# Kernel optimization log

Measured on AMD Instinct MI355X. Metric: run time of the kernel, lower is better.

Reference implementation:

```python
import jax, jax.numpy as jnp
import numpy as np

NEG_BIG = -9.0e15  # matches torch's -9000000000000000.0 mask fill
ALPHA = 0.2        # LeakyReLU negative slope


def setup_inputs() -> dict:
    key = jax.random.key(0)
    k1, k2, k3, k4 = jax.random.split(key, 4)
    bs, N, F_in, F_out = 4, 4096, 512, 64
    x = jax.random.normal(k1, (bs, N, F_in), dtype=jnp.float32)
    adj = jax.random.randint(k2, (N, N), 0, 2, dtype=jnp.int32)
    # xavier_uniform with gain=1.414
    lim_W = 1.414 * np.sqrt(6.0 / (F_in + F_out))
    W = jax.random.uniform(k3, (F_in, F_out), minval=-lim_W, maxval=lim_W, dtype=jnp.float32)
    lim_a = 1.414 * np.sqrt(6.0 / (2 * F_out + 1))
    a = jax.random.uniform(k4, (2 * F_out, 1), minval=-lim_a, maxval=lim_a, dtype=jnp.float32)
    return {"x": x, "adj": adj, "W": W, "a": a}


def reference(x, adj, W, a):
    # h = x @ W : [bs, N, F_out]
    h = jnp.einsum('bnf,fo->bno', x, W)
    F_out = W.shape[1]
    a1, a2 = a[:F_out, 0], a[F_out:, 0]  # each [F_out]
    # e_ij = LeakyReLU(a1.Wh_i + a2.Wh_j) -- same math as the O(N^2*2F) concat
    s1 = jnp.einsum('bno,o->bn', h, a1)  # [bs, N]
    s2 = jnp.einsum('bno,o->bn', h, a2)  # [bs, N]
    e = s1[:, :, None] + s2[:, None, :]  # [bs, N, N]
    e = jax.nn.leaky_relu(e, negative_slope=ALPHA)
    mask = (adj > 0)[None, :, :]
    attention = jnp.where(mask, e, NEG_BIG)
    attention = jax.nn.softmax(attention, axis=-1)
    # dropout is identity in eval mode (p applied only during training)
    h_prime = jnp.einsum('bij,bjo->bio', attention, h)
    return jax.nn.elu(h_prime)  # concat=True path
```

## Files before the change

kernel.cpp:

```cpp
#include <hip/hip_runtime.h>

#define LOG2E 1.4426950408889634f

typedef __attribute__((ext_vector_type(8))) short short8;
typedef __attribute__((ext_vector_type(4))) float f32x4;
using u32 = unsigned int;
using u16 = unsigned short;
using u64 = unsigned long long;

__global__ __launch_bounds__(256) void prep_kernel(const int* __restrict__ adj,
                                                   u32* __restrict__ mask_t,
                                                   const float* __restrict__ W,
                                                   u16* __restrict__ wt) {
    if (blockIdx.x >= 2048) {
        int t = (blockIdx.x - 2048) * 256 + threadIdx.x;
        int n = t >> 7, k4 = (t & 127) << 2;
        u32 c0 = __float_as_uint(W[(size_t)(k4 + 0) * 64 + n]) + 0x8000u;
        u32 c1 = __float_as_uint(W[(size_t)(k4 + 1) * 64 + n]) + 0x8000u;
        u32 c2 = __float_as_uint(W[(size_t)(k4 + 2) * 64 + n]) + 0x8000u;
        u32 c3 = __float_as_uint(W[(size_t)(k4 + 3) * 64 + n]) + 0x8000u;
        uint2 o;
        o.x = (c0 >> 16) | (c1 & 0xffff0000u);
        o.y = (c2 >> 16) | (c3 & 0xffff0000u);
        *(uint2*)(wt + (size_t)n * 512 + k4) = o;
        return;
    }
    const int wid = (blockIdx.x * 256 + threadIdx.x) >> 6;
    const int lane = threadIdx.x & 63;
    for (int t = wid; t < 65536; t += 8192) {
        const int r = t >> 4, c4 = t & 15;
        const int* base = adj + (size_t)r * 4096 + c4 * 256 + lane;
        int v0 = __builtin_nontemporal_load(base);
        int v1 = __builtin_nontemporal_load(base + 64);
        int v2 = __builtin_nontemporal_load(base + 128);
        int v3 = __builtin_nontemporal_load(base + 192);
        u64 b0 = __ballot(v0 > 0);
        u64 b1 = __ballot(v1 > 0);
        u64 b2 = __ballot(v2 > 0);
        u64 b3 = __ballot(v3 > 0);
        if (lane < 8) {
            u64 bv = (lane & 4) ? ((lane & 2) ? b3 : b2) : ((lane & 2) ? b1 : b0);
            u32 w = (u32)(bv >> ((lane & 1) << 5));
            mask_t[(size_t)(c4 * 8 + lane) * 4096 + r] = w;
        }
    }
}

__global__ __launch_bounds__(512) void k1f(const float* __restrict__ x,
                                           const u16* __restrict__ wt,
                                           const float* __restrict__ a,
                                           u16* __restrict__ h_t,
                                           float* __restrict__ s1p,
                                           float* __restrict__ s2p) {
    __shared__ float red[4][16][65];
    const int rt = blockIdx.x, b = blockIdx.y;
    const int tid = threadIdx.x, wave = tid >> 6, lane = tid & 63;
    const int g = wave & 3, kz = wave >> 2;
    const int m = lane & 15, quad = lane >> 4;
    const int row = rt * 64 + g * 16 + m;
    const float* xb = x + ((size_t)b * 4096 + row) * 512 + kz * 256 + quad * 8;
    const u16* wb = wt + (size_t)m * 512 + kz * 256 + quad * 8;

    f32x4 acc[4];
#pragma unroll
    for (int ot = 0; ot < 4; ot++) acc[ot] = (f32x4){0.f, 0.f, 0.f, 0.f};

    union BU { uint4 q; short8 v; };
    float4 ax[2][2];
    BU bw[2][4];
#pragma unroll
    for (int s = 0; s < 2; s++) {
        ax[s][0] = *(const float4*)(xb + s * 32);
        ax[s][1] = *(const float4*)(xb + s * 32 + 4);
#pragma unroll
        for (int ot = 0; ot < 4; ot++)
            bw[s][ot].q = *(const uint4*)(wb + (size_t)ot * 16 * 512 + s * 32);
    }
#pragma unroll
    for (int s = 0; s < 8; s++) {
        const int cur = s & 1;
        union { u32 u[4]; short8 v; } af;
        const float* a0 = (const float*)&ax[cur][0];
#pragma unroll
        for (int p = 0; p < 4; p++) {
            u32 lo = __float_as_uint(a0[2 * p]) + 0x8000u;
            u32 hi = __float_as_uint(a0[2 * p + 1]) + 0x8000u;
            af.u[p] = __builtin_amdgcn_perm(hi, lo, 0x07060302u);
        }
#pragma unroll
        for (int ot = 0; ot < 4; ot++)
            acc[ot] = __builtin_amdgcn_mfma_f32_16x16x32_bf16(af.v, bw[cur][ot].v,
                                                              acc[ot], 0, 0, 0);
        if (s + 2 < 8) {
            ax[cur][0] = *(const float4*)(xb + (s + 2) * 32);
            ax[cur][1] = *(const float4*)(xb + (s + 2) * 32 + 4);
#pragma unroll
            for (int ot = 0; ot < 4; ot++)
                bw[cur][ot].q =
                    *(const uint4*)(wb + (size_t)ot * 16 * 512 + (s + 2) * 32);
        }
    }
    if (kz) {
#pragma unroll
        for (int ot = 0; ot < 4; ot++)
#pragma unroll
            for (int r = 0; r < 4; r++)
                red[g][quad * 4 + r][ot * 16 + m] = acc[ot][r];
    }
    __syncthreads();
    if (kz) return;
#pragma unroll
    for (int ot = 0; ot < 4; ot++)
#pragma unroll
        for (int r = 0; r < 4; r++)
            acc[ot][r] += red[g][quad * 4 + r][ot * 16 + m];

    float a1v[4], a2v[4];
#pragma unroll
    for (int ot = 0; ot < 4; ot++) {
        a1v[ot] = a[ot * 16 + m];
        a2v[ot] = a[64 + ot * 16 + m];
    }
    float s1r[4], s2r[4];
#pragma unroll
    for (int r = 0; r < 4; r++) {
        s1r[r] = 0.f; s2r[r] = 0.f;
#pragma unroll
        for (int ot = 0; ot < 4; ot++) {
            s1r[r] = fmaf(acc[ot][r], a1v[ot], s1r[r]);
            s2r[r] = fmaf(acc[ot][r], a2v[ot], s2r[r]);
        }
    }
#pragma unroll
    for (int d = 1; d < 16; d <<= 1) {
#pragma unroll
        for (int r = 0; r < 4; r++) {
            s1r[r] += __shfl_xor(s1r[r], d);
            s2r[r] += __shfl_xor(s2r[r], d);
        }
    }
    if (m == 0) {
#pragma unroll
        for (int r = 0; r < 4; r++) {
            int rr = rt * 64 + g * 16 + quad * 4 + r;
            s1p[b * 4096 + rr] = s1r[r] * LOG2E;
            s2p[b * 4096 + rr] = s2r[r] * LOG2E;
        }
    }
#pragma unroll
    for (int ot = 0; ot < 4; ot++) {
        u32 b0 = __float_as_uint(acc[ot][0]) + 0x8000u;
        u32 b1 = __float_as_uint(acc[ot][1]) + 0x8000u;
        u32 b2 = __float_as_uint(acc[ot][2]) + 0x8000u;
        u32 b3 = __float_as_uint(acc[ot][3]) + 0x8000u;
        uint2 u;
        u.x = (b0 >> 16) | (b1 & 0xffff0000u);
        u.y = (b2 >> 16) | (b3 & 0xffff0000u);
        *(uint2*)(h_t + ((size_t)(b * 64 + ot * 16 + m)) * 4096
                  + rt * 64 + g * 16 + quad * 4) = u;
    }
}

template <int NSTEP>
__global__ __launch_bounds__(256, 8) void k2_attn(const u16* __restrict__ h_t,
                                                  const u32* __restrict__ mask_t,
                                                  const float* __restrict__ s1p,
                                                  const float* __restrict__ s2p,
                                                  u16* __restrict__ part,
                                                  float* __restrict__ lp) {
    constexpr int JSEG = NSTEP * 32;
    constexpr int T = NSTEP / 2;
    __shared__ u16 hB[2][64 * 64];
    __shared__ float s2l[JSEG];
    const int b = blockIdx.y, seg = blockIdx.z, rb = blockIdx.x;
    const int tid = threadIdx.x, wave = tid >> 6, lane = tid & 63;
    const int m = lane & 15, quad = lane >> 4;
    const int row = rb * 64 + wave * 16 + m;
    const int jstart = seg * JSEG;
    const float t1 = s1p[b * 4096 + row];
    const u16* hsrc = h_t + (size_t)b * 64 * 4096 + jstart;
    const u32* mrow = mask_t + (size_t)(jstart >> 5) * 4096 + row;

    for (int t = tid; t < (JSEG >> 2); t += 256)
        ((float4*)s2l)[t] = ((const float4*)(s2p + b * 4096 + jstart))[t];

    f32x4 acc[4], accd;
#pragma unroll
    for (int ot = 0; ot < 4; ot++) acc[ot] = (f32x4){0.f, 0.f, 0.f, 0.f};
    accd = (f32x4){0.f, 0.f, 0.f, 0.f};

    u32 mw[4];
#pragma unroll
    for (int s = 0; s < 4; s++) mw[s] = mrow[(size_t)s * 4096];
    union { u32 u[4]; short8 v; } ones;
#pragma unroll
    for (int p = 0; p < 4; p++) ones.u[p] = 0x3F803F80u;

    const int cj = tid & 7;
    const int ow = tid >> 3;
    uint4 pf[2];
    pf[0] = *(const uint4*)(hsrc + (size_t)ow * 4096 + (cj << 3));
    pf[1] = *(const uint4*)(hsrc + (size_t)(ow + 32) * 4096 + (cj << 3));
    *(uint4*)(hB[0] + (size_t)ow * 64 + ((cj ^ (ow & 7)) << 3)) = pf[0];
    *(uint4*)(hB[0] + (size_t)(ow + 32) * 64 + ((cj ^ ((ow + 32) & 7)) << 3)) = pf[1];
    __syncthreads();

    for (int jt = 0; jt < T; jt++) {
        const int cb = jt & 1;
        if (jt + 1 < T) {
            pf[0] = *(const uint4*)(hsrc + (size_t)ow * 4096 + (jt + 1) * 64 + (cj << 3));
            pf[1] = *(const uint4*)(hsrc + (size_t)(ow + 32) * 4096 + (jt + 1) * 64 + (cj << 3));
        }
#pragma unroll
        for (int ks = 0; ks < 2; ks++) {
            const int s = jt * 2 + ks;
            const u32 mws = mw[s & 3] >> (quad * 8);
            if (s + 4 < NSTEP) mw[(s + 4) & 3] = mrow[(size_t)(s + 4) * 4096];

            const float4 sa = *(const float4*)&s2l[s * 32 + quad * 8];
            const float4 sb = *(const float4*)&s2l[s * 32 + quad * 8 + 4];
            const float sv[8] = {sa.x, sa.y, sa.z, sa.w, sb.x, sb.y, sb.z, sb.w};
            union { u32 u[4]; short8 v; } af;
#pragma unroll
            for (int p = 0; p < 4; p++) {
                float t0 = t1 + sv[2 * p];
                float u0 = fmaxf(t0, 0.2f * t0);
                float w0 = __builtin_amdgcn_exp2f(u0);
                u32 m0 = (u32)(((int)(mws << (31 - 2 * p))) >> 31);
                u32 w0u = __float_as_uint(w0) & m0;
                float t2 = t1 + sv[2 * p + 1];
                float u2 = fmaxf(t2, 0.2f * t2);
                float w1 = __builtin_amdgcn_exp2f(u2);
                u32 m1 = (u32)(((int)(mws << (30 - 2 * p))) >> 31);
                u32 w1u = __float_as_uint(w1) & m1;
                af.u[p] = __builtin_amdgcn_perm(w1u, w0u, 0x07060302u);
            }
            const int jc = ks * 4 + quad;
#pragma unroll
            for (int ot = 0; ot < 4; ot++) {
                const int o = ot * 16 + m;
                short8 bfv = *(const short8*)(hB[cb] + (size_t)o * 64 + ((jc ^ (o & 7)) << 3));
                acc[ot] = __builtin_amdgcn_mfma_f32_16x16x32_bf16(af.v, bfv, acc[ot], 0, 0, 0);
            }
            accd = __builtin_amdgcn_mfma_f32_16x16x32_bf16(af.v, ones.v, accd, 0, 0, 0);
        }
        if (jt + 1 < T) {
            const int nb = cb ^ 1;
            *(uint4*)(hB[nb] + (size_t)ow * 64 + ((cj ^ (ow & 7)) << 3)) = pf[0];
            *(uint4*)(hB[nb] + (size_t)(ow + 32) * 64 + ((cj ^ ((ow + 32) & 7)) << 3)) = pf[1];
        }
        __syncthreads();
    }
    u16* pb = part + (((size_t)(seg * 4 + b) * 4096) + rb * 64 + wave * 16) * 64;
#pragma unroll
    for (int ot = 0; ot < 4; ot++)
#pragma unroll
        for (int r = 0; r < 4; r++) {
            u32 v = __float_as_uint(acc[ot][r]) + 0x8000u;
            pb[(quad * 4 + r) * 64 + ot * 16 + m] = (u16)(v >> 16);
        }
    if (m == 0) {
        float* lpb = lp + (size_t)(seg * 4 + b) * 4096 + rb * 64 + wave * 16 + quad * 4;
#pragma unroll
        for (int r = 0; r < 4; r++) lpb[r] = accd[r];
    }
}

template <int S>
__global__ __launch_bounds__(256) void k3_fin(const u16* __restrict__ part,
                                              const float* __restrict__ lp,
                                              float* __restrict__ out) {
    int idx = blockIdx.x * 256 + threadIdx.x;
    int o4 = (idx & 15) << 2;
    int bi = idx >> 4;
    uint2 pv[S];
    float lv[S];
#pragma unroll
    for (int s = 0; s < S; s++) {
        pv[s] = *(const uint2*)&part[((size_t)s * 16384 + bi) * 64 + o4];
        lv[s] = lp[(size_t)s * 16384 + bi];
    }
    float p0 = 0.f, p1 = 0.f, p2 = 0.f, p3 = 0.f, l = 0.f;
#pragma unroll
    for (int s = 0; s < S; s++) {
        p0 += __uint_as_float(pv[s].x << 16);
        p1 += __uint_as_float(pv[s].x & 0xffff0000u);
        p2 += __uint_as_float(pv[s].y << 16);
        p3 += __uint_as_float(pv[s].y & 0xffff0000u);
        l += lv[s];
    }
    float rl = 1.f / l;
    p0 *= rl; p1 *= rl; p2 *= rl; p3 *= rl;
    float4 o;
    o.x = p0 > 0.f ? p0 : __builtin_amdgcn_exp2f(p0 * LOG2E) - 1.f;
    o.y = p1 > 0.f ? p1 : __builtin_amdgcn_exp2f(p1 * LOG2E) - 1.f;
    o.z = p2 > 0.f ? p2 : __builtin_amdgcn_exp2f(p2 * LOG2E) - 1.f;
    o.w = p3 > 0.f ? p3 : __builtin_amdgcn_exp2f(p3 * LOG2E) - 1.f;
    *(float4*)&out[(size_t)bi * 64 + o4] = o;
}

extern "C" void kernel_launch(void* const* d_in, const int* in_sizes, int n_in,
                              void* d_out, int out_size, void* d_ws, size_t ws_size,
                              hipStream_t stream) {
    const float* x  = (const float*)d_in[0];
    const int* adj  = (const int*)d_in[1];
    const float* W  = (const float*)d_in[2];
    const float* a  = (const float*)d_in[3];
    float* out = (float*)d_out;
    char* ws = (char*)d_ws;

    u16* h_t   = (u16*)ws;
    u32* maskt = (u32*)(ws + (2 << 20));
    float* s1p = (float*)(ws + (4 << 20));
    float* s2p = s1p + 16384;
    float* lp  = s2p + 16384;
    size_t base = (4u << 20) + 2 * 65536;
    int S = 8;
    while (S > 1 && base + (size_t)S * (65536 + 2097152) + 65536 > ws_size) S >>= 1;
    u16* part = (u16*)(ws + base + (size_t)S * 65536);
    u16* wtp = (u16*)(ws + base + (size_t)S * 65536 + (size_t)S * 2097152);

    prep_kernel<<<2080, 256, 0, stream>>>(adj, maskt, W, wtp);
    k1f<<<dim3(64, 4), 512, 0, stream>>>(x, wtp, a, h_t, s1p, s2p);
    if (S == 8)      k2_attn<16><<<dim3(64, 4, 8), 256, 0, stream>>>(h_t, maskt, s1p, s2p, part, lp);
    else if (S == 4) k2_attn<32><<<dim3(64, 4, 4), 256, 0, stream>>>(h_t, maskt, s1p, s2p, part, lp);
    else if (S == 2) k2_attn<64><<<dim3(64, 4, 2), 256, 0, stream>>>(h_t, maskt, s1p, s2p, part, lp);
    else             k2_attn<128><<<dim3(64, 4, 1), 256, 0, stream>>>(h_t, maskt, s1p, s2p, part, lp);
    if (S == 8)      k3_fin<8><<<1024, 256, 0, stream>>>(part, lp, out);
    else if (S == 4) k3_fin<4><<<1024, 256, 0, stream>>>(part, lp, out);
    else if (S == 2) k3_fin<2><<<1024, 256, 0, stream>>>(part, lp, out);
    else             k3_fin<1><<<1024, 256, 0, stream>>>(part, lp, out);
}
```

Baseline: 161.6 us.

## Fuse prep with projection GEMM and fold split-K finalize into attention via tickets

Merges the adjacency mask packing, the W bf16 conversion and the x@W projection into a single kernel. Each block now computes one 16-column slice of h from a swizzled LDS copy of W, writing partial s1/s2 scores per column quarter. The separate finalize kernel is removed: the last attention segment block for each row tile, chosen by an atomic ticket counter, sums the partials, normalises and applies ELU. This cuts two launches and overlaps the mask work with the GEMM, at the cost of redundant W loads per block, four-way partial reads of s1/s2, and a serialized tail in the last-arriving blocks.

```diff
diff --git a/kernel.cpp b/kernel.cpp
--- a/kernel.cpp
+++ b/kernel.cpp
@@ -8,76 +8,69 @@
 using u16 = unsigned short;
 using u64 = unsigned long long;
 
-__global__ __launch_bounds__(256) void prep_kernel(const int* __restrict__ adj,
-                                                   u32* __restrict__ mask_t,
-                                                   const float* __restrict__ W,
-                                                   u16* __restrict__ wt) {
-    if (blockIdx.x >= 2048) {
-        int t = (blockIdx.x - 2048) * 256 + threadIdx.x;
-        int n = t >> 7, k4 = (t & 127) << 2;
-        u32 c0 = __float_as_uint(W[(size_t)(k4 + 0) * 64 + n]) + 0x8000u;
-        u32 c1 = __float_as_uint(W[(size_t)(k4 + 1) * 64 + n]) + 0x8000u;
-        u32 c2 = __float_as_uint(W[(size_t)(k4 + 2) * 64 + n]) + 0x8000u;
-        u32 c3 = __float_as_uint(W[(size_t)(k4 + 3) * 64 + n]) + 0x8000u;
-        uint2 o;
-        o.x = (c0 >> 16) | (c1 & 0xffff0000u);
-        o.y = (c2 >> 16) | (c3 & 0xffff0000u);
-        *(uint2*)(wt + (size_t)n * 512 + k4) = o;
+__global__ __launch_bounds__(256, 8) void fused_prep(
+        const float* __restrict__ x, const int* __restrict__ adj,
+        const float* __restrict__ W, const float* __restrict__ a,
+        u16* __restrict__ h_t, u32* __restrict__ mask_t,
+        float* __restrict__ s1part, float* __restrict__ s2part,
+        int* __restrict__ cnt) {
+    __shared__ u16 wq[16 * 512];
+    const int bx = blockIdx.x;
+    const int tid = threadIdx.x;
+
+    if (bx >= 1024) {
+        if (bx == 1024 && tid < 256) cnt[tid] = 0;
+        const int wid = ((bx - 1024) << 2) + (tid >> 6);
+        const int lane = tid & 63;
+        for (int t = wid; t < 65536; t += 4096) {
+            const int r = t >> 4, c4 = t & 15;
+            const int* base = adj + (size_t)r * 4096 + c4 * 256 + lane;
+            int v0 = __builtin_nontemporal_load(base);
+            int v1 = __builtin_nontemporal_load(base + 64);
+            int v2 = __builtin_nontemporal_load(base + 128);
+            int v3 = __builtin_nontemporal_load(base + 192);
+            u64 b0 = __ballot(v0 > 0);
+            u64 b1 = __ballot(v1 > 0);
+            u64 b2 = __ballot(v2 > 0);
+            u64 b3 = __ballot(v3 > 0);
+            if (lane < 8) {
+                u64 bv = (lane & 4) ? ((lane & 2) ? b3 : b2) : ((lane & 2) ? b1 : b0);
+                u32 w = (u32)(bv >> ((lane & 1) << 5));
+                mask_t[(size_t)(c4 * 8 + lane) * 4096 + r] = w;
+            }
+        }
         return;
     }
-    const int wid = (blockIdx.x * 256 + threadIdx.x) >> 6;
-    const int lane = threadIdx.x & 63;
-    for (int t = wid; t < 65536; t += 8192) {
-        const int r = t >> 4, c4 = t & 15;
-        const int* base = adj + (size_t)r * 4096 + c4 * 256 + lane;
-        int v0 = __builtin_nontemporal_load(base);
-        int v1 = __builtin_nontemporal_load(base + 64);
-        int v2 = __builtin_nontemporal_load(base + 128);
-        int v3 = __builtin_nontemporal_load(base + 192);
-        u64 b0 = __ballot(v0 > 0);
-        u64 b1 = __ballot(v1 > 0);
-        u64 b2 = __ballot(v2 > 0);
-        u64 b3 = __ballot(v3 > 0);
-        if (lane < 8) {
-            u64 bv = (lane & 4) ? ((lane & 2) ? b3 : b2) : ((lane & 2) ? b1 : b0);
-            u32 w = (u32)(bv >> ((lane & 1) << 5));
-            mask_t[(size_t)(c4 * 8 + lane) * 4096 + r] = w;
-        }
-    }
-}
-
-__global__ __launch_bounds__(512) void k1f(const float* __restrict__ x,
-                                           const u16* __restrict__ wt,
-                                           const float* __restrict__ a,
-                                           u16* __restrict__ h_t,
-                                           float* __restrict__ s1p,
-                                           float* __restrict__ s2p) {
-    __shared__ float red[4][16][65];
-    const int rt = blockIdx.x, b = blockIdx.y;
-    const int tid = threadIdx.x, wave = tid >> 6, lane = tid & 63;
-    const int g = wave & 3, kz = wave >> 2;
+
+    const int wave = tid >> 6, lane = tid & 63;
     const int m = lane & 15, quad = lane >> 4;
-    const int row = rt * 64 + g * 16 + m;
-    const float* xb = x + ((size_t)b * 4096 + row) * 512 + kz * 256 + quad * 8;
-    const u16* wb = wt + (size_t)m * 512 + kz * 256 + quad * 8;
-
-    f32x4 acc[4];
-#pragma unroll
-    for (int ot = 0; ot < 4; ot++) acc[ot] = (f32x4){0.f, 0.f, 0.f, 0.f};
-
-    union BU { uint4 q; short8 v; };
+    const int rb64 = bx & 255, oq = bx >> 8;
+
+    {
+        const int n_l = tid & 15, kg = tid >> 4;
+        const float* wsrc = W + (size_t)(kg * 32) * 64 + oq * 16 + n_l;
+#pragma unroll
+        for (int kk = 0; kk < 32; kk += 2) {
+            u32 c0 = __float_as_uint(wsrc[(size_t)kk * 64]) + 0x8000u;
+            u32 c1 = __float_as_uint(wsrc[(size_t)(kk + 1) * 64]) + 0x8000u;
+            int k = kg * 32 + kk;
+            int c = k >> 3;
+            *(u32*)&wq[n_l * 512 + ((c ^ (n_l & 7)) << 3) + (k & 7)] =
+                (c0 >> 16) | (c1 & 0xffff0000u);
+        }
+    }
+    __syncthreads();
+
+    const int row = rb64 * 64 + wave * 16 + m;
+    const float* xb = x + (size_t)row * 512 + quad * 8;
+    f32x4 acc = (f32x4){0.f, 0.f, 0.f, 0.f};
     float4 ax[2][2];
-    BU bw[2][4];
-#pragma unroll
-    for (int s = 0; s < 2; s++) {
-        ax[s][0] = *(const float4*)(xb + s * 32);
-        ax[s][1] = *(const float4*)(xb + s * 32 + 4);
-#pragma unroll
-        for (int ot = 0; ot < 4; ot++)
-            bw[s][ot].q = *(const uint4*)(wb + (size_t)ot * 16 * 512 + s * 32);
-    }
-#pragma unroll
-    for (int s = 0; s < 8; s++) {
+    ax[0][0] = *(const float4*)(xb);
+    ax[0][1] = *(const float4*)(xb + 4);
+    ax[1][0] = *(const float4*)(xb + 32);
+    ax[1][1] = *(const float4*)(xb + 36);
+#pragma unroll
+    for (int s = 0; s < 16; s++) {
         const int cur = s & 1;
         union { u32 u[4]; short8 v; } af;
         const float* a0 = (const float*)&ax[cur][0];
@@ -87,50 +80,19 @@
             u32 hi = __float_as_uint(a0[2 * p + 1]) + 0x8000u;
             af.u[p] = __builtin_amdgcn_perm(hi, lo, 0x07060302u);
         }
-#pragma unroll
-        for (int ot = 0; ot < 4; ot++)
-            acc[ot] = __builtin_amdgcn_mfma_f32_16x16x32_bf16(af.v, bw[cur][ot].v,
-                                                              acc[ot], 0, 0, 0);
-        if (s + 2 < 8) {
+        const int c = s * 4 + quad;
+        short8 bf = *(const short8*)&wq[m * 512 + ((c ^ (m & 7)) << 3)];
+        acc = __builtin_amdgcn_mfma_f32_16x16x32_bf16(af.v, bf, acc, 0, 0, 0);
+        if (s + 2 < 16) {
             ax[cur][0] = *(const float4*)(xb + (s + 2) * 32);
             ax[cur][1] = *(const float4*)(xb + (s + 2) * 32 + 4);
-#pragma unroll
-            for (int ot = 0; ot < 4; ot++)
-                bw[cur][ot].q =
-                    *(const uint4*)(wb + (size_t)ot * 16 * 512 + (s + 2) * 32);
-        }
-    }
-    if (kz) {
-#pragma unroll
-        for (int ot = 0; ot < 4; ot++)
-#pragma unroll
-            for (int r = 0; r < 4; r++)
-                red[g][quad * 4 + r][ot * 16 + m] = acc[ot][r];
-    }
-    __syncthreads();
-    if (kz) return;
-#pragma unroll
-    for (int ot = 0; ot < 4; ot++)
-#pragma unroll
-        for (int r = 0; r < 4; r++)
-            acc[ot][r] += red[g][quad * 4 + r][ot * 16 + m];
-
-    float a1v[4], a2v[4];
-#pragma unroll
-    for (int ot = 0; ot < 4; ot++) {
-        a1v[ot] = a[ot * 16 + m];
-        a2v[ot] = a[64 + ot * 16 + m];
-    }
+        }
+    }
+
+    const float a1v = a[oq * 16 + m], a2v = a[64 + oq * 16 + m];
     float s1r[4], s2r[4];
 #pragma unroll
-    for (int r = 0; r < 4; r++) {
-        s1r[r] = 0.f; s2r[r] = 0.f;
-#pragma unroll
-        for (int ot = 0; ot < 4; ot++) {
-            s1r[r] = fmaf(acc[ot][r], a1v[ot], s1r[r]);
-            s2r[r] = fmaf(acc[ot][r], a2v[ot], s2r[r]);
-        }
-    }
+    for (int r = 0; r < 4; r++) { s1r[r] = acc[r] * a1v; s2r[r] = acc[r] * a2v; }
 #pragma unroll
     for (int d = 1; d < 16; d <<= 1) {
 #pragma unroll
@@ -142,47 +104,62 @@
     if (m == 0) {
 #pragma unroll
         for (int r = 0; r < 4; r++) {
-            int rr = rt * 64 + g * 16 + quad * 4 + r;
-            s1p[b * 4096 + rr] = s1r[r] * LOG2E;
-            s2p[b * 4096 + rr] = s2r[r] * LOG2E;
-        }
-    }
-#pragma unroll
-    for (int ot = 0; ot < 4; ot++) {
-        u32 b0 = __float_as_uint(acc[ot][0]) + 0x8000u;
-        u32 b1 = __float_as_uint(acc[ot][1]) + 0x8000u;
-        u32 b2 = __float_as_uint(acc[ot][2]) + 0x8000u;
-        u32 b3 = __float_as_uint(acc[ot][3]) + 0x8000u;
-        uint2 u;
-        u.x = (b0 >> 16) | (b1 & 0xffff0000u);
-        u.y = (b2 >> 16) | (b3 & 0xffff0000u);
-        *(uint2*)(h_t + ((size_t)(b * 64 + ot * 16 + m)) * 4096
-                  + rt * 64 + g * 16 + quad * 4) = u;
-    }
+            int rr = rb64 * 64 + wave * 16 + quad * 4 + r;
+            s1part[oq * 16384 + rr] = s1r[r] * LOG2E;
+            s2part[oq * 16384 + rr] = s2r[r] * LOG2E;
+        }
+    }
+    const int bb = rb64 >> 6, rb6 = rb64 & 63;
+    u32 b0 = __float_as_uint(acc[0]) + 0x8000u;
+    u32 b1 = __float_as_uint(acc[1]) + 0x8000u;
+    u32 b2 = __float_as_uint(acc[2]) + 0x8000u;
+    u32 b3 = __float_as_uint(acc[3]) + 0x8000u;
+    uint2 u;
+    u.x = (b0 >> 16) | (b1 & 0xffff0000u);
+    u.y = (b2 >> 16) | (b3 & 0xffff0000u);
+    *(uint2*)(h_t + ((size_t)(bb * 64 + oq * 16 + m)) * 4096
+              + rb6 * 64 + wave * 16 + quad * 4) = u;
 }
 
 template <int NSTEP>
 __global__ __launch_bounds__(256, 8) void k2_attn(const u16* __restrict__ h_t,
                                                   const u32* __restrict__ mask_t,
-                                                  const float* __restrict__ s1p,
-                                                  const float* __restrict__ s2p,
+                                                  const float* __restrict__ s1part,
+                                                  const float* __restrict__ s2part,
                                                   u16* __restrict__ part,
-                                                  float* __restrict__ lp) {
+                                                  float* __restrict__ lp,
+                                                  int* __restrict__ cnt,
+                                                  float* __restrict__ out) {
     constexpr int JSEG = NSTEP * 32;
     constexpr int T = NSTEP / 2;
+    constexpr int NSEG = 128 / NSTEP;
     __shared__ u16 hB[2][64 * 64];
     __shared__ float s2l[JSEG];
+    __shared__ int ticket;
     const int b = blockIdx.y, seg = blockIdx.z, rb = blockIdx.x;
     const int tid = threadIdx.x, wave = tid >> 6, lane = tid & 63;
     const int m = lane & 15, quad = lane >> 4;
     const int row = rb * 64 + wave * 16 + m;
     const int jstart = seg * JSEG;
-    const float t1 = s1p[b * 4096 + row];
+    const int ri = b * 4096 + row;
+    const float t1 = s1part[ri] + s1part[16384 + ri]
+                   + s1part[32768 + ri] + s1part[49152 + ri];
     const u16* hsrc = h_t + (size_t)b * 64 * 4096 + jstart;
     const u32* mrow = mask_t + (size_t)(jstart >> 5) * 4096 + row;
 
-    for (int t = tid; t < (JSEG >> 2); t += 256)
-        ((float4*)s2l)[t] = ((const float4*)(s2p + b * 4096 + jstart))[t];
+    const float* s2b = s2part + b * 4096 + jstart;
+    for (int t = tid; t < (JSEG >> 2); t += 256) {
+        float4 v0 = ((const float4*)s2b)[t];
+        float4 v1 = ((const float4*)(s2b + 16384))[t];
+        float4 v2 = ((const float4*)(s2b + 32768))[t];
+        float4 v3 = ((const float4*)(s2b + 49152))[t];
+        float4 o;
+        o.x = (v0.x + v1.x) + (v2.x + v3.x);
+        o.y = (v0.y + v1.y) + (v2.y + v3.y);
+        o.z = (v0.z + v1.z) + (v2.z + v3.z);
+        o.w = (v0.w + v1.w) + (v2.w + v3.w);
+        ((float4*)s2l)[t] = o;
+    }
 
     f32x4 acc[4], accd;
 #pragma unroll
@@ -264,39 +241,50 @@
 #pragma unroll
         for (int r = 0; r < 4; r++) lpb[r] = accd[r];
     }
-}
-
-template <int S>
-__global__ __launch_bounds__(256) void k3_fin(const u16* __restrict__ part,
-                                              const float* __restrict__ lp,
-                                              float* __restrict__ out) {
-    int idx = blockIdx.x * 256 + threadIdx.x;
-    int o4 = (idx & 15) << 2;
-    int bi = idx >> 4;
-    uint2 pv[S];
-    float lv[S];
-#pragma unroll
-    for (int s = 0; s < S; s++) {
-        pv[s] = *(const uint2*)&part[((size_t)s * 16384 + bi) * 64 + o4];
-        lv[s] = lp[(size_t)s * 16384 + bi];
-    }
-    float p0 = 0.f, p1 = 0.f, p2 = 0.f, p3 = 0.f, l = 0.f;
-#pragma unroll
-    for (int s = 0; s < S; s++) {
-        p0 += __uint_as_float(pv[s].x << 16);
-        p1 += __uint_as_float(pv[s].x & 0xffff0000u);
-        p2 += __uint_as_float(pv[s].y << 16);
-        p3 += __uint_as_float(pv[s].y & 0xffff0000u);
-        l += lv[s];
-    }
-    float rl = 1.f / l;
-    p0 *= rl; p1 *= rl; p2 *= rl; p3 *= rl;
-    float4 o;
-    o.x = p0 > 0.f ? p0 : __builtin_amdgcn_exp2f(p0 * LOG2E) - 1.f;
-    o.y = p1 > 0.f ? p1 : __builtin_amdgcn_exp2f(p1 * LOG2E) - 1.f;
-    o.z = p2 > 0.f ? p2 : __builtin_amdgcn_exp2f(p2 * LOG2E) - 1.f;
-    o.w = p3 > 0.f ? p3 : __builtin_amdgcn_exp2f(p3 * LOG2E) - 1.f;
-    *(float4*)&out[(size_t)bi * 64 + o4] = o;
+
+    __threadfence();
+    __syncthreads();
+    if (tid == 0)
+        ticket = __hip_atomic_fetch_add(&cnt[(b << 6) | rb], 1,
+                                        __ATOMIC_ACQ_REL, __HIP_MEMORY_SCOPE_AGENT);
+    __syncthreads();
+    if (ticket != NSEG - 1) return;
+    __threadfence();
+
+    const int row_l = tid >> 2;
+    const int oq = tid & 3;
+    const int frow = rb * 64 + row_l;
+    float l = 0.f;
+    float po[16];
+#pragma unroll
+    for (int i = 0; i < 16; i++) po[i] = 0.f;
+#pragma unroll
+    for (int s = 0; s < NSEG; s++) {
+        const u16* ps = part + (((size_t)(s * 4 + b) * 4096) + frow) * 64 + oq * 16;
+        uint4 q0 = *(const uint4*)ps;
+        uint4 q1 = *(const uint4*)(ps + 8);
+        const u32 w0[4] = {q0.x, q0.y, q0.z, q0.w};
+        const u32 w1[4] = {q1.x, q1.y, q1.z, q1.w};
+#pragma unroll
+        for (int i = 0; i < 4; i++) {
+            po[2 * i]     += __uint_as_float(w0[i] << 16);
+            po[2 * i + 1] += __uint_as_float(w0[i] & 0xffff0000u);
+            po[8 + 2 * i]     += __uint_as_float(w1[i] << 16);
+            po[8 + 2 * i + 1] += __uint_as_float(w1[i] & 0xffff0000u);
+        }
+        l += lp[(size_t)(s * 4 + b) * 4096 + frow];
+    }
+    const float rl = 1.f / l;
+    float ov[16];
+#pragma unroll
+    for (int i = 0; i < 16; i++) {
+        float p = po[i] * rl;
+        ov[i] = p > 0.f ? p : __builtin_amdgcn_exp2f(p * LOG2E) - 1.f;
+    }
+    float* ob = out + ((size_t)(b * 4096 + frow)) * 64 + oq * 16;
+#pragma unroll
+    for (int i = 0; i < 4; i++)
+        *(float4*)(ob + i * 4) = *(float4*)&ov[i * 4];
 }
 
 extern "C" void kernel_launch(void* const* d_in, const int* in_sizes, int n_in,
@@ -309,25 +297,24 @@
     float* out = (float*)d_out;
     char* ws = (char*)d_ws;
 
-    u16* h_t   = (u16*)ws;
-    u32* maskt = (u32*)(ws + (2 << 20));
-    float* s1p = (float*)(ws + (4 << 20));
-    float* s2p = s1p + 16384;
-    float* lp  = s2p + 16384;
-    size_t base = (4u << 20) + 2 * 65536;
+    u16* h_t      = (u16*)ws;
+    u32* maskt    = (u32*)(ws + (2 << 20));
+    float* s1part = (float*)(ws + (4 << 20));
+    float* s2part = s1part + 4 * 16384;
+    size_t base = (4u << 20) + 2 * 262144;
     int S = 8;
-    while (S > 1 && base + (size_t)S * (65536 + 2097152) + 65536 > ws_size) S >>= 1;
+    while (S > 1 && base + (size_t)S * (65536 + 2097152) + 1024 > ws_size) S >>= 1;
+    float* lp = (float*)(ws + base);
     u16* part = (u16*)(ws + base + (size_t)S * 65536);
-    u16* wtp = (u16*)(ws + base + (size_t)S * 65536 + (size_t)S * 2097152);
-
-    prep_kernel<<<2080, 256, 0, stream>>>(adj, maskt, W, wtp);
-    k1f<<<dim3(64, 4), 512, 0, stream>>>(x, wtp, a, h_t, s1p, s2p);
-    if (S == 8)      k2_attn<16><<<dim3(64, 4, 8), 256, 0, stream>>>(h_t, maskt, s1p, s2p, part, lp);
-    else if (S == 4) k2_attn<32><<<dim3(64, 4, 4), 256, 0, stream>>>(h_t, maskt, s1p, s2p, part, lp);
-    else if (S == 2) k2_attn<64><<<dim3(64, 4, 2), 256, 0, stream>>>(h_t, maskt, s1p, s2p, part, lp);
-    else             k2_attn<128><<<dim3(64, 4, 1), 256, 0, stream>>>(h_t, maskt, s1p, s2p, part, lp);
-    if (S == 8)      k3_fin<8><<<1024, 256, 0, stream>>>(part, lp, out);
-    else if (S == 4) k3_fin<4><<<1024, 256, 0, stream>>>(part, lp, out);
-    else if (S == 2) k3_fin<2><<<1024, 256, 0, stream>>>(part, lp, out);
-    else             k3_fin<1><<<1024, 256, 0, stream>>>(part, lp, out);
+    int* cnt  = (int*)(ws + base + (size_t)S * (65536 + 2097152));
+
+    fused_prep<<<2048, 256, 0, stream>>>(x, adj, W, a, h_t, maskt, s1part, s2part, cnt);
+    if (S == 8)
+        k2_attn<16><<<dim3(64, 4, 8), 256, 0, stream>>>(h_t, maskt, s1part, s2part, part, lp, cnt, out);
+    else if (S == 4)
+        k2_attn<32><<<dim3(64, 4, 4), 256, 0, stream>>>(h_t, maskt, s1part, s2part, part, lp, cnt, out);
+    else if (S == 2)
+        k2_attn<64><<<dim3(64, 4, 2), 256, 0, stream>>>(h_t, maskt, s1part, s2part, part, lp, cnt, out);
+    else
+        k2_attn<128><<<dim3(64, 4, 1), 256, 0, stream>>>(h_t, maskt, s1part, s2part, part, lp, cnt, out);
 }
```

Result: slower. 474.7 us (+193.7%).
